# Kernel tuning notes

Hardware: AMD Instinct MI355X
Metric: run time of the kernel (lower is better)

The kernel has to match this reference:

```python
import jax, jax.numpy as jnp
import numpy as np

ALPHA = 1.702  # GLU sigmoid scale
LIMIT = 7.0    # clamp limit
B, S, H, E, F, TOP_K = 2, 1024, 768, 16, 768, 4


def setup_inputs() -> dict:
    key = jax.random.key(0)
    ks = jax.random.split(key, 7)
    return {
        "hidden_states": jax.random.normal(ks[0], (B, S, H), jnp.float32),
        "router_weight": jax.random.normal(ks[1], (E, H), jnp.float32) * 0.02,
        "router_bias": jax.random.normal(ks[2], (E,), jnp.float32) * 0.02,
        "gate_up_proj": jax.random.normal(ks[3], (E, H, 2 * F), jnp.float32) * 0.02,
        "gate_up_proj_bias": jax.random.normal(ks[4], (E, 2 * F), jnp.float32) * 0.02,
        "down_proj": jax.random.normal(ks[5], (E, F, H), jnp.float32) * 0.02,
        "down_proj_bias": jax.random.normal(ks[6], (E, H), jnp.float32) * 0.02,
        "top_k": TOP_K,
    }


def reference(hidden_states, router_weight, router_bias, gate_up_proj,
              gate_up_proj_bias, down_proj, down_proj_bias, top_k):
    b, s, h = hidden_states.shape
    x = hidden_states.reshape(-1, h)                      # [T, H]
    t = x.shape[0]
    # ---- TopK router ----
    logits = x @ router_weight.T + router_bias            # [T, E]
    top_val, top_idx = jax.lax.top_k(logits, top_k)       # [T, K]
    top_val = jax.nn.softmax(top_val, axis=-1)
    router_scores = jnp.zeros_like(logits).at[
        jnp.arange(t)[:, None], top_idx].set(top_val)     # [T, E]
    # ---- Dense (all-expert) FFN, as in the reference repeat+bmm ----
    gate_up = jnp.einsum('th,ehf->etf', x, gate_up_proj) \
        + gate_up_proj_bias[:, None, :]                   # [E, T, 2F]
    gate = jnp.minimum(gate_up[..., 0::2], LIMIT)         # clamp(max=limit)
    up = jnp.clip(gate_up[..., 1::2], -LIMIT, LIMIT)
    glu = gate * jax.nn.sigmoid(gate * ALPHA)
    expert_out = jnp.einsum('etf,efh->eth', (up + 1.0) * glu, down_proj) \
        + down_proj_bias[:, None, :]                      # [E, T, H]
    expert_out = expert_out.reshape(-1, b, s, h)          # [E, B, S, H]
    w = router_scores.T.reshape(-1, b, s)[..., None]      # [E, B, S, 1]
    routed_out = (expert_out * w).sum(axis=0)             # [B, S, H]
    return routed_out, router_scores
```

## Files before the change

### kernel.cpp

```cpp
#include <hip/hip_runtime.h>
#include <hip/hip_bf16.h>

#define T_TOK 2048
#define H_DIM 768
#define E_NUM 16
#define F_DIM 768
#define TWOF 1536
#define TOPK 4
#define NASSIGN 8192
#define BM 128
#define BK 64
#define KT 12
#define NTILE 80
#define NSLOTP (NTILE * BM)
#define MAXT1 10
#define CHUNK (BM * BK)
#define WTILE (64 * BK)
#define NRTR 256

typedef __bf16 bf16x8 __attribute__((ext_vector_type(8)));
typedef unsigned short us8 __attribute__((ext_vector_type(8)));
typedef float f32x4 __attribute__((ext_vector_type(4)));

__device__ __forceinline__ unsigned short f2bf(float f) {
  unsigned u = __float_as_uint(f);
  u += 0x7FFF + ((u >> 16) & 1);
  return (unsigned short)(u >> 16);
}

__device__ __forceinline__ void gl_lds16(const unsigned short* g, unsigned short* l) {
  __builtin_amdgcn_global_load_lds(
      (const __attribute__((address_space(1))) unsigned int*)g,
      (__attribute__((address_space(3))) unsigned int*)l, 16, 0, 0);
}

__global__ __launch_bounds__(256)
void router_kernel(const float* __restrict__ x, const float* __restrict__ rw,
                   const float* __restrict__ rb, float* __restrict__ scores,
                   int* __restrict__ tk_idx, float* __restrict__ tk_w,
                   int* __restrict__ tmap, float* __restrict__ wgrp,
                   unsigned short* __restrict__ xg) {
  __shared__ float lg[8][16], sc[8][16];
  const int bid = blockIdx.x;
  const int tid = threadIdx.x;
  const int t0 = bid * 8;
  if (tid < 40) {
    tmap[bid * 40 + tid] = 0;
    wgrp[bid * 40 + tid] = 0.0f;
  }
  {
    const int tokr = tid >> 5;
    const int g0 = tid & 31;
    const float* xs = x + (size_t)(t0 + tokr) * H_DIM;
    unsigned short* xd = xg + (size_t)(t0 + tokr) * H_DIM;
    #pragma unroll
    for (int i = 0; i < 3; ++i) {
      const int gg = g0 + i * 32;
      const f32x4 a = *(const f32x4*)(xs + gg * 8);
      const f32x4 b = *(const f32x4*)(xs + gg * 8 + 4);
      us8 o;
      #pragma unroll
      for (int j = 0; j < 4; ++j) { o[j] = f2bf(a[j]); o[4 + j] = f2bf(b[j]); }
      *(us8*)&xd[gg * 8] = o;
    }
  }
  const int lane32 = tid & 31, tok = tid >> 5;
  const int e = lane32 & 15, q2 = lane32 >> 4;
  const int t = t0 + tok;
  const float* xr = x + (size_t)t * H_DIM + q2 * 384;
  const float* wr = rw + (size_t)e * H_DIM + q2 * 384;
  double a0 = 0, a1 = 0, a2 = 0, a3 = 0;
  #pragma unroll 4
  for (int h = 0; h < 384; h += 4) {
    const f32x4 xv = *(const f32x4*)(xr + h);
    const f32x4 wv = *(const f32x4*)(wr + h);
    a0 += (double)xv[0] * (double)wv[0];
    a1 += (double)xv[1] * (double)wv[1];
    a2 += (double)xv[2] * (double)wv[2];
    a3 += (double)xv[3] * (double)wv[3];
  }
  double acc = (a0 + a1) + (a2 + a3);
  acc += __shfl_xor(acc, 16, 64);
  if (q2 == 0) lg[tok][e] = (float)acc + rb[e];
  __syncthreads();
  if (lane32 == 0) {
    float v[16];
    #pragma unroll
    for (int i = 0; i < 16; ++i) { v[i] = lg[tok][i]; sc[tok][i] = 0.0f; }
    int idx[TOPK]; float val[TOPK];
    for (int k = 0; k < TOPK; ++k) {
      float best = -3.4e38f; int bi = 0;
      for (int i = 0; i < 16; ++i)
        if (v[i] > best) { best = v[i]; bi = i; }
      idx[k] = bi; val[k] = best; v[bi] = -3.4e38f;
    }
    float s = 0.0f, ev[TOPK];
    for (int k = 0; k < TOPK; ++k) { ev[k] = expf(val[k] - val[0]); s += ev[k]; }
    for (int k = 0; k < TOPK; ++k) {
      float wgt = ev[k] / s;
      sc[tok][idx[k]] = wgt;
      tk_idx[t * TOPK + k] = idx[k];
      tk_w[t * TOPK + k] = wgt;
    }
  }
  __syncthreads();
  if (tid < 128)
    scores[(size_t)(t0 + (tid >> 4)) * 16 + (tid & 15)] = sc[tid >> 4][tid & 15];
}

__global__ __launch_bounds__(256)
void group_kernel(const int* __restrict__ tk_idx, const float* __restrict__ tk_w,
                  int* __restrict__ counts, int* __restrict__ offs,
                  int* __restrict__ tmap, float* __restrict__ wgrp) {
  __shared__ int hist[256][16];
  __shared__ int seg[16][16];
  __shared__ int cnt[16], eoff[16];
  const int tid = threadIdx.x;
  int loc[16];
  #pragma unroll
  for (int e = 0; e < 16; ++e) loc[e] = 0;
  const int base = tid * 32;
  int eid[32];
  for (int i = 0; i < 32; ++i) { int e = tk_idx[base + i]; eid[i] = e; loc[e]++; }
  #pragma unroll
  for (int e = 0; e < 16; ++e) hist[tid][e] = loc[e];
  __syncthreads();
  const int s = tid >> 4, e16 = tid & 15;
  {
    int sum = 0;
    #pragma unroll
    for (int j = 0; j < 16; ++j) sum += hist[s * 16 + j][e16];
    seg[s][e16] = sum;
  }
  __syncthreads();
  if (tid < 16) {
    int run = 0;
    #pragma unroll
    for (int s2 = 0; s2 < 16; ++s2) { int t = seg[s2][tid]; seg[s2][tid] = run; run += t; }
    cnt[tid] = run;
  }
  __syncthreads();
  {
    int run = seg[s][e16];
    #pragma unroll
    for (int j = 0; j < 16; ++j) { int t = hist[s * 16 + j][e16]; hist[s * 16 + j][e16] = run; run += t; }
  }
  __syncthreads();
  if (tid == 0) {
    int acc = 0;
    for (int e = 0; e < 16; ++e) { eoff[e] = acc; acc += (cnt[e] + BM - 1) / BM * BM; }
  }
  __syncthreads();
  if (tid < 16) { counts[tid] = cnt[tid]; offs[tid] = eoff[tid]; }
  int run[16];
  #pragma unroll
  for (int e = 0; e < 16; ++e) run[e] = hist[tid][e];
  for (int i = 0; i < 32; ++i) {
    int e = eid[i];
    int slot = eoff[e] + run[e]++;
    tmap[slot] = base + i;
    wgrp[slot] = tk_w[base + i];
  }
}

__global__ __launch_bounds__(512)
void convert_w_kernel(const float* __restrict__ gup, const float* __restrict__ dwn,
                      unsigned short* __restrict__ gw, unsigned short* __restrict__ uw,
                      unsigned short* __restrict__ dw) {
  const int ft = blockIdx.x, kt = blockIdx.y, z = blockIdx.z;
  const int tid = threadIdx.x;
  const int n = tid & 63, k8 = tid >> 6;
  const int doff = n * BK + 8 * (k8 ^ (n & 7));
  __shared__ unsigned short tg[WTILE], tu[WTILE];
  if (z < 16) {
    const int e = z;
    const float* src = gup + ((size_t)(e * H_DIM + kt * 64 + k8 * 8)) * TWOF
                           + 2 * (ft * 64 + n);
    us8 g, u;
    #pragma unroll
    for (int j = 0; j < 8; ++j) {
      const float2 p = *(const float2*)(src + (size_t)j * TWOF);
      g[j] = f2bf(p.x); u[j] = f2bf(p.y);
    }
    *(us8*)&tg[doff] = g;
    *(us8*)&tu[doff] = u;
    __syncthreads();
    const size_t tb = (((size_t)e * KT + kt) * 12 + ft) * WTILE;
    *(us8*)&gw[tb + tid * 8] = *(const us8*)&tg[tid * 8];
    *(us8*)&uw[tb + tid * 8] = *(const us8*)&tu[tid * 8];
  } else {
    const int e = z - 16;
    const float* src = dwn + ((size_t)(e * F_DIM + kt * 64 + k8 * 8)) * H_DIM
                           + ft * 64 + n;
    us8 o;
    #pragma unroll
    for (int j = 0; j < 8; ++j) o[j] = f2bf(src[(size_t)j * H_DIM]);
    *(us8*)&tg[doff] = o;
    __syncthreads();
    const size_t tb = (((size_t)e * KT + kt) * 12 + ft) * WTILE;
    *(us8*)&dw[tb + tid * 8] = *(const us8*)&tg[tid * 8];
  }
}

__global__ __launch_bounds__(512)
void gemm1_kernel(const unsigned short* __restrict__ xg, const unsigned short* __restrict__ gw,
                  const unsigned short* __restrict__ uw, const float* __restrict__ gupb,
                  const int* __restrict__ counts, const int* __restrict__ offs,
                  const int* __restrict__ tmap, unsigned short* __restrict__ act) {
  const int bid = blockIdx.x;
  const int swz = (bid & 7) * 120 + (bid >> 3);
  const int ey = swz / 6, ft = swz % 6;
  const int e = ey / MAXT1, tile = ey % MAXT1;
  const int count = counts[e];
  if (tile * BM >= count) return;
  const int tileg = (offs[e] >> 7) + tile;
  const int tid = threadIdx.x;
  const int wv = tid >> 6, lane = tid & 63;
  const int ml = lane & 15, lh = lane >> 4;
  const int wm = wv >> 2, wn = wv & 3;

  __shared__ unsigned short lA[CHUNK];
  __shared__ unsigned short lBg[CHUNK];
  __shared__ unsigned short lBu[CHUNK];

  const int arow = tid >> 3;
  const int agr = (tid & 7) ^ (arow & 7);
  const int t0 = tmap[tileg * BM + arow] >> 2;
  const int t1 = tmap[tileg * BM + 64 + arow] >> 2;
  const unsigned short* a0 = xg + (size_t)t0 * H_DIM + agr * 8;
  const unsigned short* a1 = xg + (size_t)t1 * H_DIM + agr * 8;

  const unsigned short* gb = gw + ((size_t)e * KT * 12 + ft * 2) * WTILE;
  const unsigned short* ub = uw + ((size_t)e * KT * 12 + ft * 2) * WTILE;

  f32x4 accg[4][2] = {};
  f32x4 accu[4][2] = {};

  for (int kt = 0; kt < KT; ++kt) {
    const unsigned short* gs = gb + (size_t)kt * 12 * WTILE;
    const unsigned short* us = ub + (size_t)kt * 12 * WTILE;
    gl_lds16(a0 + kt * 64, &lA[tid * 8]);
    gl_lds16(a1 + kt * 64, &lA[(512 + tid) * 8]);
    gl_lds16(gs + tid * 8, &lBg[tid * 8]);
    gl_lds16(gs + (512 + tid) * 8, &lBg[(512 + tid) * 8]);
    gl_lds16(us + tid * 8, &lBu[tid * 8]);
    gl_lds16(us + (512 + tid) * 8, &lBu[(512 + tid) * 8]);
    __syncthreads();
    #pragma unroll
    for (int ks = 0; ks < 2; ++ks) {
      const int slot = ks * 4 + lh;
      bf16x8 af[4];
      #pragma unroll
      for (int mf = 0; mf < 4; ++mf) {
        const int ar = wm * 64 + mf * 16 + ml;
        af[mf] = __builtin_bit_cast(bf16x8, *(const us8*)&lA[ar * BK + 8 * (slot ^ (ar & 7))]);
      }
      #pragma unroll
      for (int nf = 0; nf < 2; ++nf) {
        const int br = wn * 32 + nf * 16 + ml;
        const int ba = (br >> 6) * WTILE + (br & 63) * BK + 8 * (slot ^ (br & 7));
        bf16x8 bg = __builtin_bit_cast(bf16x8, *(const us8*)&lBg[ba]);
        bf16x8 bu = __builtin_bit_cast(bf16x8, *(const us8*)&lBu[ba]);
        #pragma unroll
        for (int mf = 0; mf < 4; ++mf) {
          accg[mf][nf] = __builtin_amdgcn_mfma_f32_16x16x32_bf16(af[mf], bg, accg[mf][nf], 0, 0, 0);
          accu[mf][nf] = __builtin_amdgcn_mfma_f32_16x16x32_bf16(af[mf], bu, accu[mf][nf], 0, 0, 0);
        }
      }
    }
    __syncthreads();
  }
  unsigned short* tbuf = (wn & 2) ? lBg : lA;
  #pragma unroll
  for (int mf = 0; mf < 4; ++mf) {
    #pragma unroll
    for (int nf = 0; nf < 2; ++nf) {
      const int fcl = wn * 32 + nf * 16 + ml;
      const int c = fcl & 63;
      const int fc = ft * 128 + fcl;
      const float bgv = gupb[(size_t)e * TWOF + 2 * fc];
      const float buv = gupb[(size_t)e * TWOF + 2 * fc + 1];
      #pragma unroll
      for (int r = 0; r < 4; ++r) {
        const int m = wm * 64 + mf * 16 + lh * 4 + r;
        float g = accg[mf][nf][r] + bgv;
        float u = accu[mf][nf][r] + buv;
        g = fminf(g, 7.0f);
        u = fminf(fmaxf(u, -7.0f), 7.0f);
        const float glu = g / (1.0f + __expf(-1.702f * g));
        tbuf[m * BK + 8 * ((c >> 3) ^ (m & 7)) + (c & 7)] = f2bf((u + 1.0f) * glu);
      }
    }
  }
  __syncthreads();
  unsigned short* ob0 = act + ((size_t)tileg * KT + ft * 2) * CHUNK;
  unsigned short* ob1 = ob0 + CHUNK;
  #pragma unroll
  for (int i = 0; i < 2; ++i) {
    *(us8*)&ob0[(i * 512 + tid) * 8] = *(const us8*)&lA[(i * 512 + tid) * 8];
    *(us8*)&ob1[(i * 512 + tid) * 8] = *(const us8*)&lBg[(i * 512 + tid) * 8];
  }
}

__global__ __launch_bounds__(512)
void gemm2_kernel(const unsigned short* __restrict__ act, const unsigned short* __restrict__ dw,
                  const float* __restrict__ dwnb, const int* __restrict__ counts,
                  const int* __restrict__ offs, const int* __restrict__ tmap,
                  const float* __restrict__ wgrp, float* __restrict__ partial) {
  const int bid = blockIdx.x;
  const int swz = (bid & 7) * 120 + (bid >> 3);
  const int ey = swz / 6, ft = swz % 6;
  const int e = ey / MAXT1, tile = ey % MAXT1;
  const int count = counts[e];
  if (tile * BM >= count) return;
  const int off = offs[e];
  const int tileg = (off >> 7) + tile;
  const int tid = threadIdx.x;
  const int wv = tid >> 6, lane = tid & 63;
  const int ml = lane & 15, lh = lane >> 4;
  const int wm = wv >> 2, wn = wv & 3;

  __shared__ unsigned short lA[CHUNK];
  __shared__ unsigned short lB[CHUNK];

  const unsigned short* ab = act + (size_t)tileg * KT * CHUNK;
  const unsigned short* bb = dw + ((size_t)e * KT * 12 + ft * 2) * WTILE;

  f32x4 acc[4][2] = {};

  for (int kt = 0; kt < KT; ++kt) {
    const unsigned short* as = ab + kt * CHUNK;
    const unsigned short* bs = bb + (size_t)kt * 12 * WTILE;
    gl_lds16(as + tid * 8, &lA[tid * 8]);
    gl_lds16(as + (512 + tid) * 8, &lA[(512 + tid) * 8]);
    gl_lds16(bs + tid * 8, &lB[tid * 8]);
    gl_lds16(bs + (512 + tid) * 8, &lB[(512 + tid) * 8]);
    __syncthreads();
    #pragma unroll
    for (int ks = 0; ks < 2; ++ks) {
      const int slot = ks * 4 + lh;
      bf16x8 af[4];
      #pragma unroll
      for (int mf = 0; mf < 4; ++mf) {
        const int ar = wm * 64 + mf * 16 + ml;
        af[mf] = __builtin_bit_cast(bf16x8, *(const us8*)&lA[ar * BK + 8 * (slot ^ (ar & 7))]);
      }
      #pragma unroll
      for (int nf = 0; nf < 2; ++nf) {
        const int br = wn * 32 + nf * 16 + ml;
        const int ba = (br >> 6) * WTILE + (br & 63) * BK + 8 * (slot ^ (br & 7));
        bf16x8 bv = __builtin_bit_cast(bf16x8, *(const us8*)&lB[ba]);
        #pragma unroll
        for (int mf = 0; mf < 4; ++mf)
          acc[mf][nf] = __builtin_amdgcn_mfma_f32_16x16x32_bf16(af[mf], bv, acc[mf][nf], 0, 0, 0);
      }
    }
    __syncthreads();
  }
  #pragma unroll
  for (int mf = 0; mf < 4; ++mf) {
    #pragma unroll
    for (int nf = 0; nf < 2; ++nf) {
      const int hc = ft * 128 + wn * 32 + nf * 16 + ml;
      const float bias = dwnb[(size_t)e * H_DIM + hc];
      #pragma unroll
      for (int r = 0; r < 4; ++r) {
        const int m = tile * BM + wm * 64 + mf * 16 + lh * 4 + r;
        if (m < count) {
          const int slot = off + m;
          partial[(size_t)tmap[slot] * H_DIM + hc] = wgrp[slot] * (acc[mf][nf][r] + bias);
        }
      }
    }
  }
}

__global__ __launch_bounds__(256)
void reduce_kernel(const float* __restrict__ partial, float* __restrict__ out) {
  const int idx = blockIdx.x * 256 + threadIdx.x;
  const int v = idx * 4;
  const int t = v / H_DIM;
  const int h = v - t * H_DIM;
  f32x4 s = {0, 0, 0, 0};
  #pragma unroll
  for (int k = 0; k < 4; ++k) {
    const f32x4 p = *(const f32x4*)&partial[(size_t)(t * 4 + k) * H_DIM + h];
    s += p;
  }
  *(f32x4*)&out[v] = s;
}

extern "C" void kernel_launch(void* const* d_in, const int* in_sizes, int n_in,
                              void* d_out, int out_size, void* d_ws, size_t ws_size,
                              hipStream_t stream) {
  const float* x    = (const float*)d_in[0];
  const float* rw   = (const float*)d_in[1];
  const float* rb   = (const float*)d_in[2];
  const float* gup  = (const float*)d_in[3];
  const float* gupb = (const float*)d_in[4];
  const float* dwn  = (const float*)d_in[5];
  const float* dwnb = (const float*)d_in[6];
  float* out = (float*)d_out;
  float* scores = out + (size_t)T_TOK * H_DIM;

  char* w = (char*)d_ws;
  int*   tk_idx = (int*)w;            w += NASSIGN * 4;
  float* tk_w   = (float*)w;          w += NASSIGN * 4;
  int*   counts = (int*)w;            w += 64;
  int*   offs   = (int*)w;            w += 64;
  int*   tmap   = (int*)w;            w += NSLOTP * 4;
  float* wgrp   = (float*)w;          w += NSLOTP * 4;
  unsigned short* gw = (unsigned short*)w; w += (size_t)E_NUM * KT * 12 * WTILE * 2;
  unsigned short* uw = (unsigned short*)w; w += (size_t)E_NUM * KT * 12 * WTILE * 2;
  unsigned short* dw = (unsigned short*)w; w += (size_t)E_NUM * KT * 12 * WTILE * 2;
  unsigned short* xg = (unsigned short*)w; w += (size_t)T_TOK * H_DIM * 2;
  unsigned short* act = (unsigned short*)w; w += (size_t)NTILE * KT * CHUNK * 2;
  float* partial = (float*)w;         w += (size_t)NASSIGN * H_DIM * 4;

  convert_w_kernel<<<dim3(12, 12, 32), 512, 0, stream>>>(gup, dwn, gw, uw, dw);
  router_kernel<<<NRTR, 256, 0, stream>>>(x, rw, rb, scores, tk_idx, tk_w, tmap, wgrp, xg);
  group_kernel<<<1, 256, 0, stream>>>(tk_idx, tk_w, counts, offs, tmap, wgrp);
  gemm1_kernel<<<6 * E_NUM * MAXT1, 512, 0, stream>>>(
      xg, gw, uw, gupb, counts, offs, tmap, act);
  gemm2_kernel<<<6 * E_NUM * MAXT1, 512, 0, stream>>>(
      act, dw, dwnb, counts, offs, tmap, wgrp, partial);
  reduce_kernel<<<(T_TOK * H_DIM / 4) / 256, 256, 0, stream>>>(partial, out);
}
```

Measured before the change: 117.0 us.

## Fuse down-proj weight bf16 conversion into gemm2 B-tile loads

Drops the separate pre-pass that converts down_proj to a tiled bf16 buffer. gemm2 now reads the fp32 down_proj directly, packs pairs with v_cvt_pk_bf16_f32, and writes swizzled bf16 into LDS. This removes one full-weight read/write pass and a workspace buffer. In exchange each gemm2 block re-reads fp32 weights (twice the bytes), using strided scalar loads instead of async global-to-LDS copies, and the same weights are re-converted by every token tile.

```diff
diff --git a/kernel.cpp b/kernel.cpp
--- a/kernel.cpp
+++ b/kernel.cpp
@@ -20,12 +20,19 @@
 
 typedef __bf16 bf16x8 __attribute__((ext_vector_type(8)));
 typedef unsigned short us8 __attribute__((ext_vector_type(8)));
+typedef unsigned uint4v __attribute__((ext_vector_type(4)));
 typedef float f32x4 __attribute__((ext_vector_type(4)));
 
 __device__ __forceinline__ unsigned short f2bf(float f) {
   unsigned u = __float_as_uint(f);
   u += 0x7FFF + ((u >> 16) & 1);
   return (unsigned short)(u >> 16);
+}
+
+__device__ __forceinline__ unsigned cvt_pk(float lo, float hi) {
+  unsigned r;
+  asm("v_cvt_pk_bf16_f32 %0, %1, %2" : "=v"(r) : "v"(lo), "v"(hi));
+  return r;
 }
 
 __device__ __forceinline__ void gl_lds16(const unsigned short* g, unsigned short* l) {
@@ -164,42 +171,27 @@
 }
 
 __global__ __launch_bounds__(512)
-void convert_w_kernel(const float* __restrict__ gup, const float* __restrict__ dwn,
-                      unsigned short* __restrict__ gw, unsigned short* __restrict__ uw,
-                      unsigned short* __restrict__ dw) {
-  const int ft = blockIdx.x, kt = blockIdx.y, z = blockIdx.z;
+void convert_w_kernel(const float* __restrict__ gup,
+                      unsigned short* __restrict__ gw, unsigned short* __restrict__ uw) {
+  const int ft = blockIdx.x, kt = blockIdx.y, e = blockIdx.z;
   const int tid = threadIdx.x;
   const int n = tid & 63, k8 = tid >> 6;
   const int doff = n * BK + 8 * (k8 ^ (n & 7));
   __shared__ unsigned short tg[WTILE], tu[WTILE];
-  if (z < 16) {
-    const int e = z;
-    const float* src = gup + ((size_t)(e * H_DIM + kt * 64 + k8 * 8)) * TWOF
-                           + 2 * (ft * 64 + n);
-    us8 g, u;
-    #pragma unroll
-    for (int j = 0; j < 8; ++j) {
-      const float2 p = *(const float2*)(src + (size_t)j * TWOF);
-      g[j] = f2bf(p.x); u[j] = f2bf(p.y);
-    }
-    *(us8*)&tg[doff] = g;
-    *(us8*)&tu[doff] = u;
-    __syncthreads();
-    const size_t tb = (((size_t)e * KT + kt) * 12 + ft) * WTILE;
-    *(us8*)&gw[tb + tid * 8] = *(const us8*)&tg[tid * 8];
-    *(us8*)&uw[tb + tid * 8] = *(const us8*)&tu[tid * 8];
-  } else {
-    const int e = z - 16;
-    const float* src = dwn + ((size_t)(e * F_DIM + kt * 64 + k8 * 8)) * H_DIM
-                           + ft * 64 + n;
-    us8 o;
-    #pragma unroll
-    for (int j = 0; j < 8; ++j) o[j] = f2bf(src[(size_t)j * H_DIM]);
-    *(us8*)&tg[doff] = o;
-    __syncthreads();
-    const size_t tb = (((size_t)e * KT + kt) * 12 + ft) * WTILE;
-    *(us8*)&dw[tb + tid * 8] = *(const us8*)&tg[tid * 8];
-  }
+  const float* src = gup + ((size_t)(e * H_DIM + kt * 64 + k8 * 8)) * TWOF
+                         + 2 * (ft * 64 + n);
+  us8 g, u;
+  #pragma unroll
+  for (int j = 0; j < 8; ++j) {
+    const float2 p = *(const float2*)(src + (size_t)j * TWOF);
+    g[j] = f2bf(p.x); u[j] = f2bf(p.y);
+  }
+  *(us8*)&tg[doff] = g;
+  *(us8*)&tu[doff] = u;
+  __syncthreads();
+  const size_t tb = (((size_t)e * KT + kt) * 12 + ft) * WTILE;
+  *(us8*)&gw[tb + tid * 8] = *(const us8*)&tg[tid * 8];
+  *(us8*)&uw[tb + tid * 8] = *(const us8*)&tu[tid * 8];
 }
 
 __global__ __launch_bounds__(512)
@@ -303,7 +295,7 @@
 }
 
 __global__ __launch_bounds__(512)
-void gemm2_kernel(const unsigned short* __restrict__ act, const unsigned short* __restrict__ dw,
+void gemm2_kernel(const unsigned short* __restrict__ act, const float* __restrict__ dwn,
                   const float* __restrict__ dwnb, const int* __restrict__ counts,
                   const int* __restrict__ offs, const int* __restrict__ tmap,
                   const float* __restrict__ wgrp, float* __restrict__ partial) {
@@ -324,17 +316,28 @@
   __shared__ unsigned short lB[CHUNK];
 
   const unsigned short* ab = act + (size_t)tileg * KT * CHUNK;
-  const unsigned short* bb = dw + ((size_t)e * KT * 12 + ft * 2) * WTILE;
+  const int bn = tid & 127, kq = tid >> 7;
+  const float* db = dwn + (size_t)e * F_DIM * H_DIM + ft * 128 + bn;
 
   f32x4 acc[4][2] = {};
 
   for (int kt = 0; kt < KT; ++kt) {
     const unsigned short* as = ab + kt * CHUNK;
-    const unsigned short* bs = bb + (size_t)kt * 12 * WTILE;
     gl_lds16(as + tid * 8, &lA[tid * 8]);
     gl_lds16(as + (512 + tid) * 8, &lA[(512 + tid) * 8]);
-    gl_lds16(bs + tid * 8, &lB[tid * 8]);
-    gl_lds16(bs + (512 + tid) * 8, &lB[(512 + tid) * 8]);
+    #pragma unroll
+    for (int half = 0; half < 2; ++half) {
+      const int k8 = kq + half * 4;
+      const float* dsrc = db + (size_t)(kt * 64 + k8 * 8) * H_DIM;
+      uint4v dv;
+      #pragma unroll
+      for (int j = 0; j < 4; ++j) {
+        const float a = dsrc[(size_t)(2 * j) * H_DIM];
+        const float b = dsrc[(size_t)(2 * j + 1) * H_DIM];
+        dv[j] = cvt_pk(a, b);
+      }
+      *(uint4v*)&lB[bn * BK + 8 * (k8 ^ (bn & 7))] = dv;
+    }
     __syncthreads();
     #pragma unroll
     for (int ks = 0; ks < 2; ++ks) {
@@ -348,7 +351,7 @@
       #pragma unroll
       for (int nf = 0; nf < 2; ++nf) {
         const int br = wn * 32 + nf * 16 + ml;
-        const int ba = (br >> 6) * WTILE + (br & 63) * BK + 8 * (slot ^ (br & 7));
+        const int ba = br * BK + 8 * (slot ^ (br & 7));
         bf16x8 bv = __builtin_bit_cast(bf16x8, *(const us8*)&lB[ba]);
         #pragma unroll
         for (int mf = 0; mf < 4; ++mf)
@@ -412,17 +415,16 @@
   float* wgrp   = (float*)w;          w += NSLOTP * 4;
   unsigned short* gw = (unsigned short*)w; w += (size_t)E_NUM * KT * 12 * WTILE * 2;
   unsigned short* uw = (unsigned short*)w; w += (size_t)E_NUM * KT * 12 * WTILE * 2;
-  unsigned short* dw = (unsigned short*)w; w += (size_t)E_NUM * KT * 12 * WTILE * 2;
   unsigned short* xg = (unsigned short*)w; w += (size_t)T_TOK * H_DIM * 2;
   unsigned short* act = (unsigned short*)w; w += (size_t)NTILE * KT * CHUNK * 2;
   float* partial = (float*)w;         w += (size_t)NASSIGN * H_DIM * 4;
 
-  convert_w_kernel<<<dim3(12, 12, 32), 512, 0, stream>>>(gup, dwn, gw, uw, dw);
+  convert_w_kernel<<<dim3(12, 12, 16), 512, 0, stream>>>(gup, gw, uw);
   router_kernel<<<NRTR, 256, 0, stream>>>(x, rw, rb, scores, tk_idx, tk_w, tmap, wgrp, xg);
   group_kernel<<<1, 256, 0, stream>>>(tk_idx, tk_w, counts, offs, tmap, wgrp);
   gemm1_kernel<<<6 * E_NUM * MAXT1, 512, 0, stream>>>(
       xg, gw, uw, gupb, counts, offs, tmap, act);
   gemm2_kernel<<<6 * E_NUM * MAXT1, 512, 0, stream>>>(
-      act, dw, dwnb, counts, offs, tmap, wgrp, partial);
+      act, dwn, dwnb, counts, offs, tmap, wgrp, partial);
   reduce_kernel<<<(T_TOK * H_DIM / 4) / 256, 256, 0, stream>>>(partial, out);
 }
```

Result: no change. 117.0 us (+0.0%).
